# Kernel optimization log

Hardware: AMD Instinct MI355X
Metric: run time of the kernel (lower is better)

## Reference

```python
import jax, jax.numpy as jnp
from jax import lax
import numpy as np

WINDOW_SIZE = 11
SIGMA = 1.5
C1 = 0.01 ** 2
C2 = 0.03 ** 2


def _window(channel, dtype):
    # 1D gaussian, matching torch: exp(-(x - ws//2)^2 / (2*sigma^2)), normalized
    x = jnp.arange(WINDOW_SIZE, dtype=jnp.float32) - WINDOW_SIZE // 2
    g = jnp.exp(-(x ** 2) / (2.0 * SIGMA ** 2))
    g = g / g.sum()
    w2d = jnp.outer(g, g)  # [ws, ws]
    return jnp.broadcast_to(w2d, (channel, 1, WINDOW_SIZE, WINDOW_SIZE)).astype(dtype)


def _depthwise_conv(x, window, channel):
    pad = WINDOW_SIZE // 2
    return lax.conv_general_dilated(
        x, window, window_strides=(1, 1),
        padding=[(pad, pad), (pad, pad)],
        dimension_numbers=('NCHW', 'OIHW', 'NCHW'),
        feature_group_count=channel)


def setup_inputs() -> dict:
    key = jax.random.key(0)
    k1, k2 = jax.random.split(key)
    img1 = jax.random.uniform(k1, (16, 3, 512, 512), dtype=jnp.float32)
    img2 = jax.random.uniform(k2, (16, 3, 512, 512), dtype=jnp.float32)
    return {'img1': img1, 'img2': img2}


def reference(img1, img2):
    channel = img1.shape[1]
    window = _window(channel, img1.dtype)
    conv = lambda t: _depthwise_conv(t, window, channel)

    mu1 = conv(img1)
    mu2 = conv(img2)
    mu1_sq = mu1 * mu1
    mu2_sq = mu2 * mu2
    mu1_mu2 = mu1 * mu2
    sigma1_sq = conv(img1 * img1) - mu1_sq
    sigma2_sq = conv(img2 * img2) - mu2_sq
    sigma12 = conv(img1 * img2) - mu1_mu2

    cs_map = (2.0 * sigma12 + C2) / (sigma1_sq + sigma2_sq + C2)
    ssim_map = (2.0 * mu1_mu2 + C1) / (mu1_sq + mu2_sq + C1) * cs_map
    return jnp.mean(ssim_map)  # size_average=True
```

## Files before the change

kernel.cpp:

```cpp
#include <hip/hip_runtime.h>
#include <math.h>

#define IMG_H 512
#define IMG_W 512
#define NPLANES 48
#define RAD 5
#define TAPS 11
#define CHUNK 33
#define STRIP 64
#define SBUF 80

#define WAVE_FENCE_WAR()  __asm__ __volatile__("" ::: "memory")
#define WAVE_FENCE_RAW()  __asm__ __volatile__("s_waitcnt lgkmcnt(0)" ::: "memory")

struct GaussW { float w[TAPS]; };

__global__ __launch_bounds__(256, 4)
void ssim_main(const float* __restrict__ img1, const float* __restrict__ img2,
               double* __restrict__ sum_ws, GaussW gw) {
    __shared__ float2 srow[4][SBUF];
    __shared__ float wsum[4];

    const int tid  = threadIdx.x;
    const int wid  = tid >> 6;
    const int lane = tid & 63;
    const int c0   = blockIdx.x * (4 * STRIP) + wid * STRIP;
    const int y0   = blockIdx.y * CHUNK;
    const size_t pbase = (size_t)blockIdx.z * (IMG_H * IMG_W);
    const float* p1 = img1 + pbase;
    const float* p2 = img2 + pbase;
    float2* buf = srow[wid];

    float r1[TAPS], r2[TAPS], r11[TAPS], r22[TAPS], r12[TAPS];

    float pa, pb, pta, ptb;

    auto load_regs = [&](int r) {
        pa = pb = pta = ptb = 0.f;
        if (r >= 0 && r < IMG_H) {
            const float* row1 = p1 + (size_t)r * IMG_W;
            const float* row2 = p2 + (size_t)r * IMG_W;
            int col = c0 - RAD + lane;
            if (col >= 0 && col < IMG_W) { pa = row1[col]; pb = row2[col]; }
            if (lane < 2 * RAD) {
                int c2 = c0 + STRIP - RAD + lane;
                if (c2 < IMG_W) { pta = row1[c2]; ptb = row2[c2]; }
            }
        }
    };

    auto store_lds = [&]() {
        WAVE_FENCE_WAR();
        buf[lane] = make_float2(pa, pb);
        if (lane < 2 * RAD) buf[STRIP + lane] = make_float2(pta, ptb);
        WAVE_FENCE_RAW();
    };

    auto hconv = [&](int r, float& o1, float& o2, float& o11, float& o22, float& o12) {
        float a1 = 0.f, a2 = 0.f, a11 = 0.f, a22 = 0.f, a12 = 0.f;
        if (r >= 0 && r < IMG_H) {
            #pragma unroll
            for (int d = 0; d < TAPS; ++d) {
                float2 v = buf[lane + d];
                float wv = gw.w[d];
                a1  = fmaf(wv, v.x, a1);
                a2  = fmaf(wv, v.y, a2);
                a11 = fmaf(wv, v.x * v.x, a11);
                a22 = fmaf(wv, v.y * v.y, a22);
                a12 = fmaf(wv, v.x * v.y, a12);
            }
        }
        o1 = a1; o2 = a2; o11 = a11; o22 = a22; o12 = a12;
    };

    load_regs(y0 - RAD);
    #pragma unroll
    for (int k = 0; k < TAPS - 1; ++k) {
        const int r = y0 - RAD + k;
        store_lds();
        load_regs(r + 1);
        hconv(r, r1[k], r2[k], r11[k], r22[k], r12[k]);
    }

    const float C1v = 0.0001f;
    const float C2v = 0.0009f;
    float acc = 0.f;

    for (int kk = 0; kk < CHUNK; kk += TAPS) {
        #pragma unroll
        for (int j = 0; j < TAPS; ++j) {
            const int r = y0 - RAD + (TAPS - 1) + kk + j;
            store_lds();
            load_regs(r + 1);
            hconv(r, r1[(j + 10) % TAPS], r2[(j + 10) % TAPS],
                  r11[(j + 10) % TAPS], r22[(j + 10) % TAPS], r12[(j + 10) % TAPS]);

            const int y = y0 + kk + j;
            if (y < IMG_H) {
                float mu1 = 0.f, mu2 = 0.f, s11 = 0.f, s22 = 0.f, s12 = 0.f;
                #pragma unroll
                for (int t = 0; t < TAPS; ++t) {
                    const int s = (j + t) % TAPS;
                    float wv = gw.w[t];
                    mu1 = fmaf(wv, r1[s], mu1);
                    mu2 = fmaf(wv, r2[s], mu2);
                    s11 = fmaf(wv, r11[s], s11);
                    s22 = fmaf(wv, r22[s], s22);
                    s12 = fmaf(wv, r12[s], s12);
                }
                float mu1sq = mu1 * mu1, mu2sq = mu2 * mu2, mu12 = mu1 * mu2;
                float sg1 = s11 - mu1sq, sg2 = s22 - mu2sq, sg12 = s12 - mu12;
                float num = (2.f * mu12 + C1v) * (2.f * sg12 + C2v);
                float den = (mu1sq + mu2sq + C1v) * (sg1 + sg2 + C2v);
                acc += num * __builtin_amdgcn_rcpf(den);
            }
        }
    }

    #pragma unroll
    for (int off = 32; off > 0; off >>= 1) acc += __shfl_down(acc, off, 64);
    if (lane == 0) wsum[wid] = acc;
    __syncthreads();
    if (tid == 0) {
        double s = (double)wsum[0] + (double)wsum[1] + (double)wsum[2] + (double)wsum[3];
        atomicAdd(sum_ws, s);
    }
}

__global__ void ssim_finalize(const double* __restrict__ sum_ws, float* __restrict__ out) {
    out[0] = (float)(sum_ws[0] * (1.0 / (double)(16.0 * 3.0 * 512.0 * 512.0)));
}

extern "C" void kernel_launch(void* const* d_in, const int* in_sizes, int n_in,
                              void* d_out, int out_size, void* d_ws, size_t ws_size,
                              hipStream_t stream) {
    const float* img1 = (const float*)d_in[0];
    const float* img2 = (const float*)d_in[1];
    float* out = (float*)d_out;
    double* ws = (double*)d_ws;

    hipMemsetAsync(ws, 0, sizeof(double), stream);

    GaussW gw;
    double g[TAPS], s = 0.0;
    for (int i = 0; i < TAPS; ++i) {
        double x = (double)(i - TAPS / 2);
        g[i] = exp(-(x * x) / (2.0 * 1.5 * 1.5));
        s += g[i];
    }
    for (int i = 0; i < TAPS; ++i) gw.w[i] = (float)(g[i] / s);

    dim3 grid(IMG_W / (4 * STRIP), (IMG_H + CHUNK - 1) / CHUNK, NPLANES);
    ssim_main<<<grid, 256, 0, stream>>>(img1, img2, ws, gw);
    ssim_finalize<<<1, 1, 0, stream>>>(ws, out);
}
```

Before: 162.2 us.

## Switch separable SSIM convolutions to packed half2 arithmetic with centered inputs

Horizontal and vertical Gaussian passes now run in packed fp16 (half2 FMA), with each lane handling two columns 64 apart. Inputs are shifted by 0.5 before conversion to limit fp16 error, and the shift is undone analytically using per-pixel window weight sums that account for zero padding at borders. Chunk height drops to 16 rows with one block covering the full row width, which changes the halo overhead and grid shape. The aim is to halve ALU and LDS work per pixel. The cost is reduced precision in the variance terms, where fp16 cancellation could disturb the mean.

```diff
diff --git a/kernel.cpp b/kernel.cpp
--- a/kernel.cpp
+++ b/kernel.cpp
@@ -1,4 +1,5 @@
 #include <hip/hip_runtime.h>
+#include <hip/hip_fp16.h>
 #include <math.h>
 
 #define IMG_H 512
@@ -6,71 +7,91 @@
 #define NPLANES 48
 #define RAD 5
 #define TAPS 11
-#define CHUNK 33
-#define STRIP 64
+#define CHUNK 16
 #define SBUF 80
 
 #define WAVE_FENCE_WAR()  __asm__ __volatile__("" ::: "memory")
 #define WAVE_FENCE_RAW()  __asm__ __volatile__("s_waitcnt lgkmcnt(0)" ::: "memory")
 
-struct GaussW { float w[TAPS]; };
+struct GaussPk { unsigned w[TAPS]; float wf[TAPS]; };
+
+__device__ __forceinline__ unsigned h2bits(__half2 h) { return __builtin_bit_cast(unsigned, h); }
+__device__ __forceinline__ __half2  bits2h(unsigned u) { return __builtin_bit_cast(__half2, u); }
 
 __global__ __launch_bounds__(256, 4)
 void ssim_main(const float* __restrict__ img1, const float* __restrict__ img2,
-               double* __restrict__ sum_ws, GaussW gw) {
-    __shared__ float2 srow[4][SBUF];
+               double* __restrict__ sum_ws, GaussPk gw) {
+    __shared__ unsigned planes[4][2][SBUF];
     __shared__ float wsum[4];
 
     const int tid  = threadIdx.x;
     const int wid  = tid >> 6;
     const int lane = tid & 63;
-    const int c0   = blockIdx.x * (4 * STRIP) + wid * STRIP;
+    const int c0   = wid * 128;
     const int y0   = blockIdx.y * CHUNK;
     const size_t pbase = (size_t)blockIdx.z * (IMG_H * IMG_W);
     const float* p1 = img1 + pbase;
     const float* p2 = img2 + pbase;
-    float2* buf = srow[wid];
-
-    float r1[TAPS], r2[TAPS], r11[TAPS], r22[TAPS], r12[TAPS];
-
-    float pa, pb, pta, ptb;
+    unsigned* ap = planes[wid][0];
+    unsigned* bp = planes[wid][1];
+
+    const int g0 = c0 - RAD + lane;
+    const bool q0 = (g0 >= 0);
+    const int g1 = c0 + 59 + lane;
+    const int g2 = c0 + 123 + lane;
+    const bool q2 = (lane < 2 * RAD) && (g2 < IMG_W);
+
+    const int x1 = c0 + lane, x2 = c0 + 64 + lane;
+    float Wc1 = 0.f, Wc2 = 0.f;
+    #pragma unroll
+    for (int d = 0; d < TAPS; ++d) {
+        if ((unsigned)(x1 + d - RAD) < IMG_W) Wc1 += gw.wf[d];
+        if ((unsigned)(x2 + d - RAD) < IMG_W) Wc2 += gw.wf[d];
+    }
+
+    __half2 rA[TAPS], rB[TAPS], rAA[TAPS], rBB[TAPS], rAB[TAPS];
+    const __half2 hz = __float2half2_rn(0.0f);
+
+    float pa0, pa1, pa2, pb0, pb1, pb2;
 
     auto load_regs = [&](int r) {
-        pa = pb = pta = ptb = 0.f;
+        pa0 = pa1 = pa2 = pb0 = pb1 = pb2 = 0.f;
         if (r >= 0 && r < IMG_H) {
-            const float* row1 = p1 + (size_t)r * IMG_W;
-            const float* row2 = p2 + (size_t)r * IMG_W;
-            int col = c0 - RAD + lane;
-            if (col >= 0 && col < IMG_W) { pa = row1[col]; pb = row2[col]; }
-            if (lane < 2 * RAD) {
-                int c2 = c0 + STRIP - RAD + lane;
-                if (c2 < IMG_W) { pta = row1[c2]; ptb = row2[c2]; }
-            }
+            const float* r1 = p1 + (size_t)r * IMG_W;
+            const float* r2 = p2 + (size_t)r * IMG_W;
+            if (q0) { pa0 = r1[g0] - 0.5f; pb0 = r2[g0] - 0.5f; }
+            pa1 = r1[g1] - 0.5f; pb1 = r2[g1] - 0.5f;
+            if (q2) { pa2 = r1[g2] - 0.5f; pb2 = r2[g2] - 0.5f; }
         }
     };
 
     auto store_lds = [&]() {
         WAVE_FENCE_WAR();
-        buf[lane] = make_float2(pa, pb);
-        if (lane < 2 * RAD) buf[STRIP + lane] = make_float2(pta, ptb);
+        ap[lane] = h2bits(__float22half2_rn(make_float2(pa0, pa1)));
+        bp[lane] = h2bits(__float22half2_rn(make_float2(pb0, pb1)));
+        if (lane < 2 * RAD) {
+            ap[64 + lane] = h2bits(__float22half2_rn(make_float2(pa1, pa2)));
+            bp[64 + lane] = h2bits(__float22half2_rn(make_float2(pb1, pb2)));
+        }
         WAVE_FENCE_RAW();
     };
 
-    auto hconv = [&](int r, float& o1, float& o2, float& o11, float& o22, float& o12) {
-        float a1 = 0.f, a2 = 0.f, a11 = 0.f, a22 = 0.f, a12 = 0.f;
+    auto hconv = [&](int r, __half2& oA, __half2& oB, __half2& oAA, __half2& oBB, __half2& oAB) {
+        __half2 hA = hz, hB = hz, hAA = hz, hBB = hz, hAB = hz;
         if (r >= 0 && r < IMG_H) {
             #pragma unroll
             for (int d = 0; d < TAPS; ++d) {
-                float2 v = buf[lane + d];
-                float wv = gw.w[d];
-                a1  = fmaf(wv, v.x, a1);
-                a2  = fmaf(wv, v.y, a2);
-                a11 = fmaf(wv, v.x * v.x, a11);
-                a22 = fmaf(wv, v.y * v.y, a22);
-                a12 = fmaf(wv, v.x * v.y, a12);
+                __half2 va = bits2h(ap[lane + d]);
+                __half2 vb = bits2h(bp[lane + d]);
+                __half2 wv = bits2h(gw.w[d]);
+                hA  = __hfma2(wv, va, hA);
+                hB  = __hfma2(wv, vb, hB);
+                hAA = __hfma2(wv, __hmul2(va, va), hAA);
+                hBB = __hfma2(wv, __hmul2(vb, vb), hBB);
+                hAB = __hfma2(wv, __hmul2(va, vb), hAB);
             }
         }
-        o1 = a1; o2 = a2; o11 = a11; o22 = a22; o12 = a12;
+        oA = hA; oB = hB; oAA = hAA; oBB = hBB; oAB = hAB;
     };
 
     load_regs(y0 - RAD);
@@ -79,40 +100,63 @@
         const int r = y0 - RAD + k;
         store_lds();
         load_regs(r + 1);
-        hconv(r, r1[k], r2[k], r11[k], r22[k], r12[k]);
+        hconv(r, rA[k], rB[k], rAA[k], rBB[k], rAB[k]);
     }
 
     const float C1v = 0.0001f;
     const float C2v = 0.0009f;
     float acc = 0.f;
 
+    #pragma unroll
     for (int kk = 0; kk < CHUNK; kk += TAPS) {
         #pragma unroll
         for (int j = 0; j < TAPS; ++j) {
-            const int r = y0 - RAD + (TAPS - 1) + kk + j;
-            store_lds();
-            load_regs(r + 1);
-            hconv(r, r1[(j + 10) % TAPS], r2[(j + 10) % TAPS],
-                  r11[(j + 10) % TAPS], r22[(j + 10) % TAPS], r12[(j + 10) % TAPS]);
-
-            const int y = y0 + kk + j;
-            if (y < IMG_H) {
-                float mu1 = 0.f, mu2 = 0.f, s11 = 0.f, s22 = 0.f, s12 = 0.f;
+            if (kk + j < CHUNK) {
+                const int rowc = kk + j;
+                const int r = y0 + RAD + rowc;
+                store_lds();
+                load_regs(r + 1);
+                hconv(r, rA[(rowc + 10) % TAPS], rB[(rowc + 10) % TAPS],
+                      rAA[(rowc + 10) % TAPS], rBB[(rowc + 10) % TAPS],
+                      rAB[(rowc + 10) % TAPS]);
+
+                __half2 sA = hz, sB = hz, sAA = hz, sBB = hz, sAB = hz;
                 #pragma unroll
                 for (int t = 0; t < TAPS; ++t) {
-                    const int s = (j + t) % TAPS;
-                    float wv = gw.w[t];
-                    mu1 = fmaf(wv, r1[s], mu1);
-                    mu2 = fmaf(wv, r2[s], mu2);
-                    s11 = fmaf(wv, r11[s], s11);
-                    s22 = fmaf(wv, r22[s], s22);
-                    s12 = fmaf(wv, r12[s], s12);
+                    const int s = (rowc + t) % TAPS;
+                    __half2 wv = bits2h(gw.w[t]);
+                    sA  = __hfma2(wv, rA[s],  sA);
+                    sB  = __hfma2(wv, rB[s],  sB);
+                    sAA = __hfma2(wv, rAA[s], sAA);
+                    sBB = __hfma2(wv, rBB[s], sBB);
+                    sAB = __hfma2(wv, rAB[s], sAB);
                 }
-                float mu1sq = mu1 * mu1, mu2sq = mu2 * mu2, mu12 = mu1 * mu2;
-                float sg1 = s11 - mu1sq, sg2 = s22 - mu2sq, sg12 = s12 - mu12;
-                float num = (2.f * mu12 + C1v) * (2.f * sg12 + C2v);
-                float den = (mu1sq + mu2sq + C1v) * (sg1 + sg2 + C2v);
-                acc += num * __builtin_amdgcn_rcpf(den);
+
+                const int y = y0 + rowc;
+                float Wr = 0.f;
+                #pragma unroll
+                for (int t = 0; t < TAPS; ++t)
+                    if ((unsigned)(y + t - RAD) < IMG_H) Wr += gw.wf[t];
+
+                #pragma unroll
+                for (int px = 0; px < 2; ++px) {
+                    float m1  = px ? __high2float(sA)  : __low2float(sA);
+                    float m2  = px ? __high2float(sB)  : __low2float(sB);
+                    float P11 = px ? __high2float(sAA) : __low2float(sAA);
+                    float P22 = px ? __high2float(sBB) : __low2float(sBB);
+                    float P12 = px ? __high2float(sAB) : __low2float(sAB);
+                    float W   = (px ? Wc2 : Wc1) * Wr;
+                    float mu1 = fmaf(0.5f, W, m1);
+                    float mu2 = fmaf(0.5f, W, m2);
+                    float qW  = 0.25f * W;
+                    float mu1sq = mu1 * mu1, mu2sq = mu2 * mu2, mu12 = mu1 * mu2;
+                    float sg1  = P11 + mu1 - qW - mu1sq;
+                    float sg2  = P22 + mu2 - qW - mu2sq;
+                    float sg12 = P12 + 0.5f * (mu1 + mu2) - qW - mu12;
+                    float num = (2.f * mu12 + C1v) * (2.f * sg12 + C2v);
+                    float den = (mu1sq + mu2sq + C1v) * (sg1 + sg2 + C2v);
+                    acc += num * __builtin_amdgcn_rcpf(den);
+                }
             }
         }
     }
@@ -129,6 +173,18 @@
 
 __global__ void ssim_finalize(const double* __restrict__ sum_ws, float* __restrict__ out) {
     out[0] = (float)(sum_ws[0] * (1.0 / (double)(16.0 * 3.0 * 512.0 * 512.0)));
+}
+
+static unsigned short f32_to_f16_rne(float f) {
+    unsigned x; __builtin_memcpy(&x, &f, 4);
+    unsigned sign = (x >> 16) & 0x8000u;
+    int exp = (int)((x >> 23) & 0xffu) - 127 + 15;
+    unsigned man = x & 0x7fffffu;
+    if (exp <= 0) return (unsigned short)sign;
+    unsigned h = sign | ((unsigned)exp << 10) | (man >> 13);
+    unsigned rnd = man & 0x1fffu;
+    if (rnd > 0x1000u || (rnd == 0x1000u && (h & 1u))) h++;
+    return (unsigned short)h;
 }
 
 extern "C" void kernel_launch(void* const* d_in, const int* in_sizes, int n_in,
@@ -141,16 +197,21 @@
 
     hipMemsetAsync(ws, 0, sizeof(double), stream);
 
-    GaussW gw;
+    GaussPk gw;
     double g[TAPS], s = 0.0;
     for (int i = 0; i < TAPS; ++i) {
         double x = (double)(i - TAPS / 2);
         g[i] = exp(-(x * x) / (2.0 * 1.5 * 1.5));
         s += g[i];
     }
-    for (int i = 0; i < TAPS; ++i) gw.w[i] = (float)(g[i] / s);
-
-    dim3 grid(IMG_W / (4 * STRIP), (IMG_H + CHUNK - 1) / CHUNK, NPLANES);
+    for (int i = 0; i < TAPS; ++i) {
+        float wf = (float)(g[i] / s);
+        gw.wf[i] = wf;
+        unsigned short h = f32_to_f16_rne(wf);
+        gw.w[i] = (unsigned)h | ((unsigned)h << 16);
+    }
+
+    dim3 grid(1, IMG_H / CHUNK, NPLANES);
     ssim_main<<<grid, 256, 0, stream>>>(img1, img2, ws, gw);
     ssim_finalize<<<1, 1, 0, stream>>>(ws, out);
 }
```

Result: slower. 225.2 us (+38.8%).
